# Kernel tuning notes

Hardware: AMD Instinct MI355X
Metric: run time of the kernel (lower is better)

## Reference

```python
import jax, jax.numpy as jnp
import numpy as np

B, T, C = 2, 2048, 1024
H, M = 16, 64
D = C // H  # head_dim = 64


def setup_inputs() -> dict:
    key = jax.random.key(0)
    ks = jax.random.split(key, 6)
    x = jax.random.normal(ks[0], (B, T, C), dtype=jnp.float32)
    Wqkv = jax.random.normal(ks[1], (3 * C, C), dtype=jnp.float32) / np.sqrt(C)
    bqkv = jax.random.normal(ks[2], (3 * C,), dtype=jnp.float32) * 0.02
    Wout = jax.random.normal(ks[3], (C, C), dtype=jnp.float32) / np.sqrt(C)
    bout = jax.random.normal(ks[4], (C,), dtype=jnp.float32) * 0.02
    proj = jax.random.normal(ks[5], (H, D, M), dtype=jnp.float32) / np.sqrt(D)
    return {"x": x, "Wqkv": Wqkv, "bqkv": bqkv, "Wout": Wout, "bout": bout, "proj": proj}


def reference(x, Wqkv, bqkv, Wout, bout, proj):
    b, t, c = x.shape
    h, d, m = proj.shape
    qkv = x @ Wqkv.T + bqkv                          # [B,T,3C]
    q, k, v = jnp.split(qkv, 3, axis=-1)
    # [B,T,C] -> [B,H,T,D]
    to_heads = lambda z: z.reshape(b, t, h, d).transpose(0, 2, 1, 3)
    q, k, v = to_heads(q), to_heads(k), to_heads(v)
    qf, kf, vf = q.astype(jnp.float32), k.astype(jnp.float32), v.astype(jnp.float32)
    pf = proj.astype(jnp.float32)
    q_prime = jax.nn.relu(jnp.einsum('bhtd,hdm->bhtm', qf, pf))
    k_prime = jax.nn.relu(jnp.einsum('bhtd,hdm->bhtm', kf, pf))
    k_cumsum = jnp.cumsum(k_prime, axis=2)                        # [B,H,T,M]
    kv_prod = jnp.einsum('bhtm,bhtd->bhtmd', k_prime, vf)          # [B,H,T,M,D]
    kv_cumsum = jnp.cumsum(kv_prod, axis=2)                        # [B,H,T,M,D]
    context = jnp.einsum('bhtm,bhtmd->bhtd', q_prime, kv_cumsum)   # [B,H,T,D]
    norm = jnp.einsum('bhtm,bhtm->bht', q_prime, k_cumsum)         # [B,H,T]
    out = context / (norm[..., None] + 1e-6)
    out = out.astype(x.dtype).transpose(0, 2, 1, 3).reshape(b, t, c)
    return out @ Wout.T + bout
```

## Files before the change

kernel.cpp:

```cpp
#include <hip/hip_runtime.h>
#include <cstddef>

#define B_  2
#define T_  2048
#define C_  1024
#define H_  16
#define D_  64
#define M_  64
#define NC_ 32
#define CH_ 64

typedef __attribute__((ext_vector_type(8))) short bf16x8;
typedef __attribute__((ext_vector_type(4))) float f32x4;

__device__ __forceinline__ ushort f2bf(float f) {
    union { float f; unsigned u; } v; v.f = f;
    unsigned r = v.u + 0x7FFF + ((v.u >> 16) & 1);
    return (ushort)(r >> 16);
}
__device__ __forceinline__ float bf2f(ushort u) {
    union { unsigned u; float f; } x; x.u = ((unsigned)u) << 16; return x.f;
}

__device__ __forceinline__ void gld_lds16(const ushort* g, ushort* lds) {
    __builtin_amdgcn_global_load_lds(
        (const __attribute__((address_space(1))) unsigned int*)g,
        (__attribute__((address_space(3))) unsigned int*)lds,
        16, 0, 0);
}

__device__ __forceinline__ bf16x8 frag_ld(const ushort* lds, int row16, int k0, int lane) {
    int r = row16 + (lane & 15);
    int byte = ((k0 * 2) + ((lane >> 4) << 4)) ^ ((r & 7) << 4);
    return *(const bf16x8*)((const char*)lds + r * 128 + byte);
}

#define VMCNT(n) asm volatile("s_waitcnt vmcnt(" #n ")" ::: "memory")
#define BAR() do { __builtin_amdgcn_s_barrier(); __builtin_amdgcn_sched_barrier(0); } while (0)

#define SEG1_ 256
#define SEG2_ 512
#define SEG3_ 1536
#define SEG4_ 1792
#define NPREP_ 1804

__global__ __launch_bounds__(256) void prep_all(
    const float* __restrict__ x, const float* __restrict__ Wqkv,
    const float* __restrict__ bqkv, const float* __restrict__ Wout,
    const float* __restrict__ proj,
    ushort* __restrict__ Wbt, ushort* __restrict__ xbf,
    ushort* __restrict__ WoutBf, float* __restrict__ bbig)
{
    __shared__ float Ws[64 * 128];
    __shared__ float Ps[64 * 64];
    const int blk = blockIdx.x, t = threadIdx.x;
    if (blk < SEG1_) {
        const int sel = blk >> 7, h = (blk >> 3) & 15, cc = blk & 7;
        const int rowbase = sel * 1024 + h * 64;
        {
            const int r0 = t >> 5, cq = t & 31;
#pragma unroll
            for (int k = 0; k < 8; ++k) {
                int r = r0 + 8 * k;
                *(float4*)&Ws[r * 128 + cq * 4] =
                    *(const float4*)&Wqkv[(size_t)(rowbase + r) * 1024 + cc * 128 + cq * 4];
            }
        }
#pragma unroll
        for (int k = 0; k < 4; ++k) {
            int i4 = t + 256 * k;
            *(float4*)&Ps[i4 * 4] = *(const float4*)&proj[h * 4096 + i4 * 4];
        }
        __syncthreads();
#pragma unroll
        for (int k = 0; k < 2; ++k) {
            int id = t + 256 * k;
            int m4 = id >> 5, c4 = id & 31;
            float4 a0 = {0.f,0.f,0.f,0.f}, a1 = a0, a2 = a0, a3 = a0;
            for (int d = 0; d < 64; ++d) {
                float4 w = *(const float4*)&Ws[d * 128 + c4 * 4];
                float4 p = *(const float4*)&Ps[d * 64 + m4 * 4];
                a0.x += p.x*w.x; a0.y += p.x*w.y; a0.z += p.x*w.z; a0.w += p.x*w.w;
                a1.x += p.y*w.x; a1.y += p.y*w.y; a1.z += p.y*w.z; a1.w += p.y*w.w;
                a2.x += p.z*w.x; a2.y += p.z*w.y; a2.z += p.z*w.z; a2.w += p.z*w.w;
                a3.x += p.w*w.x; a3.y += p.w*w.y; a3.z += p.w*w.z; a3.w += p.w*w.w;
            }
            size_t obase = (size_t)(rowbase + m4 * 4) * 1024 + cc * 128 + c4 * 4;
            ushort4 o0 = { f2bf(a0.x), f2bf(a0.y), f2bf(a0.z), f2bf(a0.w) };
            ushort4 o1 = { f2bf(a1.x), f2bf(a1.y), f2bf(a1.z), f2bf(a1.w) };
            ushort4 o2 = { f2bf(a2.x), f2bf(a2.y), f2bf(a2.z), f2bf(a2.w) };
            ushort4 o3 = { f2bf(a3.x), f2bf(a3.y), f2bf(a3.z), f2bf(a3.w) };
            *(ushort4*)&Wbt[obase]          = o0;
            *(ushort4*)&Wbt[obase + 1024]   = o1;
            *(ushort4*)&Wbt[obase + 2048]   = o2;
            *(ushort4*)&Wbt[obase + 3072]   = o3;
        }
    } else if (blk < SEG2_) {
        int bo = blk - SEG1_;
#pragma unroll
        for (int pass = 0; pass < 4; ++pass) {
            int i4 = bo * 1024 + pass * 256 + t;
            float4 v = ((const float4*)Wqkv)[524288 + i4];
            ushort4 o = { f2bf(v.x), f2bf(v.y), f2bf(v.z), f2bf(v.w) };
            ((ushort4*)(Wbt + 2097152))[i4] = o;
        }
    } else if (blk < SEG3_) {
        int bo = blk - SEG2_;
#pragma unroll
        for (int pass = 0; pass < 4; ++pass) {
            int i4 = bo * 1024 + pass * 256 + t;
            float4 v = ((const float4*)x)[i4];
            ushort4 o = { f2bf(v.x), f2bf(v.y), f2bf(v.z), f2bf(v.w) };
            ((ushort4*)xbf)[i4] = o;
        }
    } else if (blk < SEG4_) {
        int bo = blk - SEG3_;
#pragma unroll
        for (int pass = 0; pass < 4; ++pass) {
            int i4 = bo * 1024 + pass * 256 + t;
            float4 v = ((const float4*)Wout)[i4];
            ushort4 o = { f2bf(v.x), f2bf(v.y), f2bf(v.z), f2bf(v.w) };
            ((ushort4*)WoutBf)[i4] = o;
        }
    } else {
        int j = (blk - SEG4_) * 256 + t;
        if (j < 2048) {
            int sel = j >> 10, hm = j & 1023, h = hm >> 6, m = hm & 63;
            const float* b = bqkv + sel * C_ + h * D_;
            const float* p = proj + (size_t)h * D_ * M_ + m;
            float acc = 0.f;
#pragma unroll 8
            for (int d = 0; d < D_; ++d) acc += b[d] * p[(size_t)d * M_];
            bbig[j] = acc;
        } else {
            bbig[j] = bqkv[j];
        }
    }
}

__device__ __forceinline__ void g_stage_G0(const ushort* __restrict__ Ag, const ushort* __restrict__ Bg,
                                           ushort* Abuf, ushort* Bbuf,
                                           int m0, int n0, int K, int kcol, int w, int lane) {
    const int l8 = lane >> 3, lc = (lane & 7) * 8;
    {
        int rbase = (w < 4) ? w * 8 : 64 + (w - 4) * 8;
        int r = rbase + l8;
        int cs = lc ^ ((r & 7) << 3);
        gld_lds16(Ag + (size_t)(m0 + r) * K + kcol + cs, Abuf + rbase * 64);
    }
    {
        int rbase = (w >> 1) * 32 + (w & 1) * 8;
        int r = rbase + l8;
        int cs = lc ^ ((r & 7) << 3);
        gld_lds16(Bg + (size_t)(n0 + r) * K + kcol + cs, Bbuf + rbase * 64);
    }
}

__device__ __forceinline__ void g_stage_G1(const ushort* __restrict__ Ag, const ushort* __restrict__ Bg,
                                           ushort* Abuf, ushort* Bbuf,
                                           int m0, int n0, int K, int kcol, int w, int lane) {
    const int l8 = lane >> 3, lc = (lane & 7) * 8;
    {
        int rbase = 16 + (w >> 1) * 32 + (w & 1) * 8;
        int r = rbase + l8;
        int cs = lc ^ ((r & 7) << 3);
        gld_lds16(Bg + (size_t)(n0 + r) * K + kcol + cs, Bbuf + rbase * 64);
    }
    {
        int rbase = (w < 4) ? 32 + w * 8 : 96 + (w - 4) * 8;
        int r = rbase + l8;
        int cs = lc ^ ((r & 7) << 3);
        gld_lds16(Ag + (size_t)(m0 + r) * K + kcol + cs, Abuf + rbase * 64);
    }
}

__device__ __forceinline__ void lda2(const ushort* Abuf, bf16x8 (&a)[2][2], int wr, int Mh, int lane) {
#pragma unroll
    for (int i = 0; i < 2; ++i)
#pragma unroll
        for (int ks = 0; ks < 2; ++ks)
            a[i][ks] = frag_ld(Abuf, wr + Mh * 32 + i * 16, ks * 32, lane);
}
__device__ __forceinline__ void g_ldb(const ushort* Bbuf, bf16x8 (&b)[2], int wc, int Nh, int lane) {
#pragma unroll
    for (int ks = 0; ks < 2; ++ks)
        b[ks] = frag_ld(Bbuf, wc + Nh * 16, ks * 32, lane);
}
__device__ __forceinline__ void g_mfma(f32x4 (&acc)[4][2], const bf16x8 (&a)[2][2],
                                       const bf16x8 (&b)[2], int Mh, int Nh) {
    __builtin_amdgcn_s_setprio(1);
#pragma unroll
    for (int ks = 0; ks < 2; ++ks)
#pragma unroll
        for (int i = 0; i < 2; ++i)
            acc[Mh * 2 + i][Nh] = __builtin_amdgcn_mfma_f32_16x16x32_bf16(
                a[i][ks], b[ks], acc[Mh * 2 + i][Nh], 0, 0, 0);
    __builtin_amdgcn_s_setprio(0);
}

template <bool BF16OUT>
__global__ __launch_bounds__(512, 4) void gemm_u8p(
    const ushort* __restrict__ A, const ushort* __restrict__ Bt,
    const float* __restrict__ bias, void* __restrict__ Cout,
    int M, int N, int K, int reluLimit)
{
    __shared__ __align__(16) ushort lds[32768];

    const int tid = threadIdx.x, w = tid >> 6, lane = tid & 63;
    const int m0 = blockIdx.y * 128, n0 = blockIdx.x * 128;
    const int wr = (w >> 2) * 64, wc = (w & 3) * 32;
    f32x4 acc[4][2] = {};
    const int NT = K / 64;

    g_stage_G0(A, Bt, lds, lds + 16384, m0, n0, K, 0, w, lane);
    g_stage_G1(A, Bt, lds, lds + 16384, m0, n0, K, 0, w, lane);

    for (int kt = 0; kt < NT - 1; ++kt) {
        const int p = kt & 1;
        ushort* Acur = lds + p * 8192;
        ushort* Anxt = lds + (p ^ 1) * 8192;
        ushort* Bcur = lds + 16384 + p * 8192;
        ushort* Bnxt = lds + 16384 + (p ^ 1) * 8192;
        const int kc1 = (kt + 1) * 64;
        bf16x8 a[2][2], a2[2][2], b[2], b2[2];
        VMCNT(2); BAR();
        g_stage_G0(A, Bt, Anxt, Bnxt, m0, n0, K, kc1, w, lane);
        lda2(Acur, a, wr, 0, lane);
        g_ldb(Bcur, b, wc, 0, lane);
        g_mfma(acc, a, b, 0, 0);
        VMCNT(3); BAR();
        g_ldb(Bcur, b2, wc, 1, lane);
        g_mfma(acc, a, b2, 0, 1);
        VMCNT(2); BAR();
        g_stage_G1(A, Bt, Anxt, Bnxt, m0, n0, K, kc1, w, lane);
        lda2(Acur, a2, wr, 1, lane);
        g_mfma(acc, a2, b, 1, 0);
        g_mfma(acc, a2, b2, 1, 1);
    }
    {
        const int p = (NT - 1) & 1;
        ushort* Acur = lds + p * 8192;
        ushort* Bcur = lds + 16384 + p * 8192;
        bf16x8 a[2][2], a2[2][2], b[2], b2[2];
        VMCNT(2); BAR();
        lda2(Acur, a, wr, 0, lane);
        g_ldb(Bcur, b, wc, 0, lane);
        g_mfma(acc, a, b, 0, 0);
        VMCNT(1); BAR();
        g_ldb(Bcur, b2, wc, 1, lane);
        g_mfma(acc, a, b2, 0, 1);
        VMCNT(0); BAR();
        lda2(Acur, a2, wr, 1, lane);
        g_mfma(acc, a2, b, 1, 0);
        g_mfma(acc, a2, b2, 1, 1);
    }

    const int crow = (lane >> 4) * 4, ccol = lane & 15;
#pragma unroll
    for (int nj = 0; nj < 2; ++nj) {
        int col = n0 + wc + nj * 16 + ccol;
        float bv = bias[col];
        bool rl = col < reluLimit;
#pragma unroll
        for (int mi = 0; mi < 4; ++mi) {
#pragma unroll
            for (int rr = 0; rr < 4; ++rr) {
                int row = m0 + wr + mi * 16 + crow + rr;
                float v = acc[mi][nj][rr] + bv;
                if (rl) v = fmaxf(v, 0.f);
                if (BF16OUT)
                    ((ushort*)Cout)[(size_t)row * N + col] = f2bf(v);
                else
                    ((float*)Cout)[(size_t)row * N + col] = v;
            }
        }
    }
}

__global__ __launch_bounds__(256) void chunk_kv_mfma(
    const ushort* __restrict__ out1, ushort* __restrict__ VtG,
    ushort* __restrict__ StB, float* __restrict__ sks)
{
    __shared__ unsigned Tl[64 * 76];
    __shared__ ushort Ktb[64 * 64];
    __shared__ ushort Vtb[64 * 64];
    __shared__ float skp[4][64];
    const int blk = blockIdx.x, c = blk & 31, bh = blk >> 5;
    const int b = bh >> 4, h = bh & 15, t0 = c * CH_;
    const int tid = threadIdx.x, wave = tid >> 6, lane = tid & 63;
    const ushort* kg = out1 + (size_t)(b * T_ + t0) * 3072 + C_ + h * D_;
    const ushort* vg = kg + C_;

#pragma unroll
    for (int it = 0; it < 2; ++it) {
        int i = tid + it * 256, r = i >> 3, sl = i & 7;
        bf16x8 v = *(const bf16x8*)(kg + (size_t)r * 3072 + sl * 8);
        unsigned* dst = &Tl[r * 76 + sl * 8];
        uint4 w0 = { (ushort)v[0], (ushort)v[1], (ushort)v[2], (ushort)v[3] };
        uint4 w1 = { (ushort)v[4], (ushort)v[5], (ushort)v[6], (ushort)v[7] };
        *(uint4*)dst = w0;
        *(uint4*)(dst + 4) = w1;
    }
    __syncthreads();
    {
        int m = tid >> 2, tc = tid & 3;
        bf16x8 va, vb;
        float s = 0.f;
#pragma unroll
        for (int k = 0; k < 8; ++k) {
            ushort u = (ushort)Tl[(tc * 16 + k) * 76 + m];
            va[k] = (short)u; s += bf2f(u);
        }
#pragma unroll
        for (int k = 0; k < 8; ++k) {
            ushort u = (ushort)Tl[(tc * 16 + 8 + k) * 76 + m];
            vb[k] = (short)u; s += bf2f(u);
        }
        skp[tc][m] = s;
        int b0 = (tc * 32) ^ ((m & 7) << 4);
        int b1 = (tc * 32 + 16) ^ ((m & 7) << 4);
        *(bf16x8*)((char*)Ktb + m * 128 + b0) = va;
        *(bf16x8*)((char*)Ktb + m * 128 + b1) = vb;
    }
    __syncthreads();
#pragma unroll
    for (int it = 0; it < 2; ++it) {
        int i = tid + it * 256, r = i >> 3, sl = i & 7;
        bf16x8 v = *(const bf16x8*)(vg + (size_t)r * 3072 + sl * 8);
        unsigned* dst = &Tl[r * 76 + sl * 8];
        uint4 w0 = { (ushort)v[0], (ushort)v[1], (ushort)v[2], (ushort)v[3] };
        uint4 w1 = { (ushort)v[4], (ushort)v[5], (ushort)v[6], (ushort)v[7] };
        *(uint4*)dst = w0;
        *(uint4*)(dst + 4) = w1;
    }
    __syncthreads();
    {
        int d = tid >> 2, tc = tid & 3;
        bf16x8 va, vb;
#pragma unroll
        for (int k = 0; k < 8; ++k) va[k] = (short)(ushort)Tl[(tc * 16 + k) * 76 + d];
#pragma unroll
        for (int k = 0; k < 8; ++k) vb[k] = (short)(ushort)Tl[(tc * 16 + 8 + k) * 76 + d];
        int b0 = (tc * 32) ^ ((d & 7) << 4);
        int b1 = (tc * 32 + 16) ^ ((d & 7) << 4);
        *(bf16x8*)((char*)Vtb + d * 128 + b0) = va;
        *(bf16x8*)((char*)Vtb + d * 128 + b1) = vb;
        ushort* og = VtG + (size_t)blk * 4096 + d * 64 + tc * 16;
        *(bf16x8*)og = va;
        *(bf16x8*)(og + 8) = vb;
    }
    __syncthreads();
    const int wr = wave * 16, g = lane >> 4, ccol = lane & 15;
    f32x4 acc[4] = {};
#pragma unroll
    for (int k0 = 0; k0 < 64; k0 += 32) {
        bf16x8 av = frag_ld(Vtb, wr, k0, lane);
#pragma unroll
        for (int j = 0; j < 4; ++j)
            acc[j] = __builtin_amdgcn_mfma_f32_16x16x32_bf16(av, frag_ld(Ktb, j * 16, k0, lane), acc[j], 0, 0, 0);
    }
    ushort* stg = StB + (size_t)blk * 4096;
#pragma unroll
    for (int j = 0; j < 4; ++j)
#pragma unroll
        for (int r = 0; r < 4; ++r)
            stg[(wr + g * 4 + r) * 64 + j * 16 + ccol] = f2bf(acc[j][r]);
    if (tid < 64)
        sks[(size_t)blk * 64 + tid] = skp[0][tid] + skp[1][tid] + skp[2][tid] + skp[3][tid];
}

__global__ __launch_bounds__(256) void chunk_scan2(const ushort* __restrict__ StB,
                                                   const float* __restrict__ sks,
                                                   ushort* __restrict__ Sbf,
                                                   ushort* __restrict__ skb) {
    if (blockIdx.x < 512) {
        int id = blockIdx.x * 256 + threadIdx.x;
        int bh = id >> 12, e = id & 4095;
        const ushort* p = StB + (size_t)bh * NC_ * 4096 + e;
        ushort* q = Sbf + (size_t)bh * NC_ * 4096 + e;
        float run = 0.f;
        for (int c = 0; c < NC_; ++c) {
            q[(size_t)c * 4096] = f2bf(run);
            run += bf2f(p[(size_t)c * 4096]);
        }
    } else {
        int id2 = (blockIdx.x - 512) * 256 + threadIdx.x;
        int bh = id2 >> 6, m = id2 & 63;
        const float* p = sks + (size_t)bh * NC_ * 64 + m;
        ushort* q = skb + (size_t)bh * NC_ * 64 + m;
        float run = 0.f;
        for (int c = 0; c < NC_; ++c) {
            q[c * 64] = f2bf(run);
            run += p[c * 64];
        }
    }
}

__global__ __launch_bounds__(256) void chunk_attn_mfma(
    const ushort* __restrict__ out1, const ushort* __restrict__ VtG,
    const ushort* __restrict__ Sbf, const ushort* __restrict__ skb,
    ushort* __restrict__ attnBf)
{
    __shared__ ushort Ql[64 * 64];
    __shared__ ushort Kl[64 * 64];
    __shared__ ushort Vl[64 * 64];
    __shared__ ushort Al[64 * 64];
    __shared__ ushort Sl[80 * 64];
    const int blk = blockIdx.x, c = blk & 31, bh = blk >> 5;
    const int b = bh >> 4, h = bh & 15, t0 = c * CH_;
    const int tid = threadIdx.x, wave = tid >> 6, lane = tid & 63;
    const ushort* qg  = out1 + (size_t)(b * T_ + t0) * 3072 + h * D_;
    const ushort* kg  = qg + C_;
    const ushort* vtg = VtG + (size_t)blk * 4096;
    const ushort* sbg = Sbf + (size_t)blk * 4096;
#pragma unroll
    for (int it = 0; it < 2; ++it) {
        int i = tid + it * 256, r = i >> 3, sl = i & 7;
        int lo = (sl * 16) ^ ((r & 7) << 4);
        *(bf16x8*)((char*)Ql + r * 128 + lo) = *(const bf16x8*)(qg + (size_t)r * 3072 + sl * 8);
        *(bf16x8*)((char*)Kl + r * 128 + lo) = *(const bf16x8*)(kg + (size_t)r * 3072 + sl * 8);
        *(bf16x8*)((char*)Vl + r * 128 + lo) = *(const bf16x8*)(vtg + r * 64 + sl * 8);
        *(bf16x8*)((char*)Sl + r * 128 + lo) = *(const bf16x8*)(sbg + r * 64 + sl * 8);
    }
    if (tid < 8)
        *(bf16x8*)((char*)Sl + 64 * 128 + tid * 16) = *(const bf16x8*)(skb + (size_t)blk * 64 + tid * 8);
    __syncthreads();

    const int wr = wave * 16, g = lane >> 4, ccol = lane & 15;
    f32x4 accA[4] = {};
#pragma unroll
    for (int k0 = 0; k0 < 64; k0 += 32) {
        bf16x8 aq = frag_ld(Ql, wr, k0, lane);
#pragma unroll
        for (int j = 0; j < 4; ++j)
            accA[j] = __builtin_amdgcn_mfma_f32_16x16x32_bf16(aq, frag_ld(Kl, j * 16, k0, lane), accA[j], 0, 0, 0);
    }
    float rsum[4] = {0.f, 0.f, 0.f, 0.f};
#pragma unroll
    for (int j = 0; j < 4; ++j) {
#pragma unroll
        for (int r = 0; r < 4; ++r) {
            int tl = wr + g * 4 + r, sl2 = j * 16 + ccol;
            float v = (sl2 <= tl) ? accA[j][r] : 0.f;
            rsum[r] += v;
            *(ushort*)((char*)Al + tl * 128 + ((sl2 * 2) ^ ((tl & 7) << 4))) = f2bf(v);
        }
    }
#pragma unroll
    for (int r = 0; r < 4; ++r) {
        rsum[r] += __shfl_xor(rsum[r], 1);
        rsum[r] += __shfl_xor(rsum[r], 2);
        rsum[r] += __shfl_xor(rsum[r], 4);
        rsum[r] += __shfl_xor(rsum[r], 8);
    }
    f32x4 accC[4] = {};
    f32x4 accE = {};
#pragma unroll
    for (int k0 = 0; k0 < 64; k0 += 32) {
        bf16x8 aa = frag_ld(Al, wr, k0, lane);
#pragma unroll
        for (int j = 0; j < 4; ++j)
            accC[j] = __builtin_amdgcn_mfma_f32_16x16x32_bf16(aa, frag_ld(Vl, j * 16, k0, lane), accC[j], 0, 0, 0);
    }
#pragma unroll
    for (int k0 = 0; k0 < 64; k0 += 32) {
        bf16x8 aq = frag_ld(Ql, wr, k0, lane);
#pragma unroll
        for (int j = 0; j < 4; ++j)
            accC[j] = __builtin_amdgcn_mfma_f32_16x16x32_bf16(aq, frag_ld(Sl, j * 16, k0, lane), accC[j], 0, 0, 0);
        accE = __builtin_amdgcn_mfma_f32_16x16x32_bf16(aq, frag_ld(Sl, 64, k0, lane), accE, 0, 0, 0);
    }
    ushort* og = attnBf + (size_t)(b * T_ + t0) * C_ + h * D_;
#pragma unroll
    for (int r = 0; r < 4; ++r) {
        float nq = __shfl(accE[r], (lane & 48));
        float inv = 1.f / (nq + rsum[r] + 1e-6f);
        int tl = wr + g * 4 + r;
#pragma unroll
        for (int j = 0; j < 4; ++j)
            og[(size_t)tl * C_ + j * 16 + ccol] = f2bf(accC[j][r] * inv);
    }
}

extern "C" void kernel_launch(void* const* d_in, const int* in_sizes, int n_in,
                              void* d_out, int out_size, void* d_ws, size_t ws_size,
                              hipStream_t stream) {
    (void)in_sizes; (void)n_in; (void)out_size; (void)ws_size;
    const float* x    = (const float*)d_in[0];
    const float* Wqkv = (const float*)d_in[1];
    const float* bqkv = (const float*)d_in[2];
    const float* Wout = (const float*)d_in[3];
    const float* bout = (const float*)d_in[4];
    const float* proj = (const float*)d_in[5];
    float* out = (float*)d_out;
    char* ws = (char*)d_ws;

    ushort* Wbt    = (ushort*)(ws);
    ushort* xbf    = (ushort*)(ws + (6ull  << 20));
    ushort* WoutBf = (ushort*)(ws + (14ull << 20));
    ushort* attnBf = (ushort*)(ws + (16ull << 20));
    float*  bbig   = (float*) (ws + (24ull << 20));
    ushort* out1   = (ushort*)(ws + (25ull << 20));
    ushort* VtG    = (ushort*)(ws + (49ull << 20));
    ushort* StB    = (ushort*)(ws + (57ull << 20));
    ushort* Sbf    = (ushort*)(ws + (65ull << 20));
    float*  sks    = (float*) (ws + (73ull << 20));
    ushort* skb    = (ushort*)(ws + (74ull << 20));

    prep_all<<<NPREP_, 256, 0, stream>>>(x, Wqkv, bqkv, Wout, proj,
                                         Wbt, xbf, WoutBf, bbig);
    gemm_u8p<true><<<dim3(24, 32), 512, 0, stream>>>(xbf, Wbt, bbig, out1,
                                                     4096, 3072, 1024, 2048);
    chunk_kv_mfma<<<1024, 256, 0, stream>>>(out1, VtG, StB, sks);
    chunk_scan2<<<520, 256, 0, stream>>>(StB, sks, Sbf, skb);
    chunk_attn_mfma<<<1024, 256, 0, stream>>>(out1, VtG, Sbf, skb, attnBf);
    gemm_u8p<false><<<dim3(8, 32), 512, 0, stream>>>(attnBf, WoutBf, bout, out,
                                                     4096, 1024, 1024, 0);
}
```

Baseline: 86.76 us.

## Use 256x256-tile GEMM kernel for QKV projection

Adds a new GEMM kernel with 256x256 output tiles (8 waves, each computing 128x64) for the first QKV projection, launched as a 12x16 grid instead of 24x32 blocks of 128x128. Larger tiles raise arithmetic intensity per LDS load and global fetch. The price is 128 KB of LDS and a large accumulator register footprint, which allows only about 2 blocks per CU, and the 192 blocks may underfill the GPU's CUs. The second GEMM is de-templated into a float-output variant with the relu removed.

```diff
diff --git a/kernel.cpp b/kernel.cpp
--- a/kernel.cpp
+++ b/kernel.cpp
@@ -138,6 +138,109 @@
     }
 }
 
+__device__ __forceinline__ void g1_stage(const ushort* __restrict__ G, ushort* buf,
+                                         int base0, int K, int kcol, int unit, int w, int lane) {
+    int rb = unit * 64 + w * 8;
+    int r  = rb + (lane >> 3);
+    int c  = (lane & 7) * 8;
+    int cs = c ^ ((r & 7) << 3);
+    gld_lds16(G + (size_t)(base0 + r) * K + kcol + cs, buf + rb * 64);
+}
+
+__device__ __forceinline__ void g1_lda(const ushort* Abuf, bf16x8 (&a)[4][2], int row0, int lane) {
+#pragma unroll
+    for (int i = 0; i < 4; ++i)
+#pragma unroll
+        for (int ks = 0; ks < 2; ++ks)
+            a[i][ks] = frag_ld(Abuf, row0 + i * 16, ks * 32, lane);
+}
+__device__ __forceinline__ void g1_ldb(const ushort* Bbuf, bf16x8 (&b)[2][2], int row0, int lane) {
+#pragma unroll
+    for (int j = 0; j < 2; ++j)
+#pragma unroll
+        for (int ks = 0; ks < 2; ++ks)
+            b[j][ks] = frag_ld(Bbuf, row0 + j * 16, ks * 32, lane);
+}
+__device__ __forceinline__ void g1_mfma(f32x4 (&acc)[8][4], const bf16x8 (&a)[4][2],
+                                        const bf16x8 (&b)[2][2], int Mh, int Nh) {
+    __builtin_amdgcn_s_setprio(1);
+#pragma unroll
+    for (int ks = 0; ks < 2; ++ks)
+#pragma unroll
+        for (int i = 0; i < 4; ++i)
+#pragma unroll
+            for (int j = 0; j < 2; ++j)
+                acc[Mh * 4 + i][Nh * 2 + j] = __builtin_amdgcn_mfma_f32_16x16x32_bf16(
+                    a[i][ks], b[j][ks], acc[Mh * 4 + i][Nh * 2 + j], 0, 0, 0);
+    __builtin_amdgcn_s_setprio(0);
+}
+
+__global__ __launch_bounds__(512, 2) void gemm1_256(
+    const ushort* __restrict__ A, const ushort* __restrict__ Bt,
+    const float* __restrict__ bias, ushort* __restrict__ Cout,
+    int M, int N, int K, int reluLimit)
+{
+    __shared__ __align__(16) ushort lds[65536];
+
+    const int tid = threadIdx.x, w = tid >> 6, lane = tid & 63;
+    const int m0 = blockIdx.y * 256, n0 = blockIdx.x * 256;
+    const int wr = (w >> 2) * 128, wc = (w & 3) * 64;
+    f32x4 acc[8][4] = {};
+    const int NT = K / 64;
+
+#pragma unroll
+    for (int u = 0; u < 4; ++u) g1_stage(A,  lds,         m0, K, 0, u, w, lane);
+#pragma unroll
+    for (int u = 0; u < 4; ++u) g1_stage(Bt, lds + 32768, n0, K, 0, u, w, lane);
+
+    for (int kt = 0; kt < NT; ++kt) {
+        const int p = kt & 1;
+        ushort* Acur = lds + p * 16384;
+        ushort* Bcur = lds + 32768 + p * 16384;
+        ushort* Anxt = lds + (p ^ 1) * 16384;
+        ushort* Bnxt = lds + 32768 + (p ^ 1) * 16384;
+        const int kc1 = (kt + 1) * 64;
+        const bool pf = (kt + 1) < NT;
+        bf16x8 a0[4][2], a1[4][2], b0[2][2], b1[2][2];
+
+        VMCNT(0); BAR();
+        if (pf) { g1_stage(A, Anxt, m0, K, kc1, 0, w, lane);
+                  g1_stage(A, Anxt, m0, K, kc1, 1, w, lane); }
+        g1_lda(Acur, a0, wr, lane);
+        g1_ldb(Bcur, b0, wc, lane);
+        g1_mfma(acc, a0, b0, 0, 0);
+        if (pf) { g1_stage(A, Anxt, m0, K, kc1, 2, w, lane);
+                  g1_stage(A, Anxt, m0, K, kc1, 3, w, lane); }
+        g1_ldb(Bcur, b1, wc + 32, lane);
+        g1_mfma(acc, a0, b1, 0, 1);
+        if (pf) { g1_stage(Bt, Bnxt, n0, K, kc1, 0, w, lane);
+                  g1_stage(Bt, Bnxt, n0, K, kc1, 1, w, lane); }
+        g1_lda(Acur, a1, wr + 64, lane);
+        g1_mfma(acc, a1, b0, 1, 0);
+        if (pf) { g1_stage(Bt, Bnxt, n0, K, kc1, 2, w, lane);
+                  g1_stage(Bt, Bnxt, n0, K, kc1, 3, w, lane); }
+        g1_mfma(acc, a1, b1, 1, 1);
+    }
+
+    const int crow = (lane >> 4) * 4, ccol = lane & 15;
+#pragma unroll
+    for (int nj = 0; nj < 4; ++nj) {
+        int col = n0 + wc + nj * 16 + ccol;
+        float bv = bias[col];
+        bool rl = col < reluLimit;
+#pragma unroll
+        for (int mi = 0; mi < 8; ++mi) {
+#pragma unroll
+            for (int rr = 0; rr < 4; ++rr) {
+                int row = m0 + wr + mi * 16 + crow + rr;
+                float v = acc[mi][nj][rr] + bv;
+                if (rl) v = fmaxf(v, 0.f);
+                Cout[(size_t)row * N + col] = f2bf(v);
+            }
+        }
+    }
+}
+
 __device__ __forceinline__ void g_stage_G0(const ushort* __restrict__ Ag, const ushort* __restrict__ Bg,
                                            ushort* Abuf, ushort* Bbuf,
                                            int m0, int n0, int K, int kcol, int w, int lane) {
@@ -198,11 +301,10 @@
     __builtin_amdgcn_s_setprio(0);
 }
 
-template <bool BF16OUT>
-__global__ __launch_bounds__(512, 4) void gemm_u8p(
+__global__ __launch_bounds__(512, 4) void gemm2_8phase(
     const ushort* __restrict__ A, const ushort* __restrict__ Bt,
-    const float* __restrict__ bias, void* __restrict__ Cout,
-    int M, int N, int K, int reluLimit)
+    const float* __restrict__ bias, float* __restrict__ Cout,
+    int M, int N, int K)
 {
     __shared__ __align__(16) ushort lds[32768];
 
@@ -260,18 +362,12 @@
     for (int nj = 0; nj < 2; ++nj) {
         int col = n0 + wc + nj * 16 + ccol;
         float bv = bias[col];
-        bool rl = col < reluLimit;
 #pragma unroll
         for (int mi = 0; mi < 4; ++mi) {
 #pragma unroll
             for (int rr = 0; rr < 4; ++rr) {
                 int row = m0 + wr + mi * 16 + crow + rr;
-                float v = acc[mi][nj][rr] + bv;
-                if (rl) v = fmaxf(v, 0.f);
-                if (BF16OUT)
-                    ((ushort*)Cout)[(size_t)row * N + col] = f2bf(v);
-                else
-                    ((float*)Cout)[(size_t)row * N + col] = v;
+                Cout[(size_t)row * N + col] = acc[mi][nj][rr] + bv;
             }
         }
     }
@@ -509,11 +605,11 @@
 
     prep_all<<<NPREP_, 256, 0, stream>>>(x, Wqkv, bqkv, Wout, proj,
                                          Wbt, xbf, WoutBf, bbig);
-    gemm_u8p<true><<<dim3(24, 32), 512, 0, stream>>>(xbf, Wbt, bbig, out1,
-                                                     4096, 3072, 1024, 2048);
+    gemm1_256<<<dim3(12, 16), 512, 0, stream>>>(xbf, Wbt, bbig, out1,
+                                                4096, 3072, 1024, 2048);
     chunk_kv_mfma<<<1024, 256, 0, stream>>>(out1, VtG, StB, sks);
     chunk_scan2<<<520, 256, 0, stream>>>(StB, sks, Sbf, skb);
     chunk_attn_mfma<<<1024, 256, 0, stream>>>(out1, VtG, Sbf, skb, attnBf);
-    gemm_u8p<false><<<dim3(8, 32), 512, 0, stream>>>(attnBf, WoutBf, bout, out,
-                                                     4096, 1024, 1024, 0);
-}
+    gemm2_8phase<<<dim3(8, 32), 512, 0, stream>>>(attnBf, WoutBf, bout, out,
+                                                  4096, 1024, 1024);
+}
```

Measured after the change: 87.58 us. About the same (+1.0%).
